# Kernel optimization log

Measured on AMD Instinct MI355X. Metric: run time of the kernel, lower is better.

## Reference

```python
import jax, jax.numpy as jnp
import numpy as np

# Static sizes
B, P, D = 256, 32, 128            # graphs, patches/graph, hidden
N, NS = 200_000, 500_000          # original nodes, combined-subgraph nodes
ES, EO = 1_000_000, 400_000       # combined-subgraph edges, original edges
RW, PRW = 20, 8                   # rw_dim, patch_rw_dim
NL_GNN, NL_MIX = 4, 2
TH, CH = 64, 512                  # mixer token-hidden, channel-hidden
ATOM_V, BOND_V = 128, 8


def seg_sum(x, idx, n):
    return jax.ops.segment_sum(x, idx, num_segments=n)


def seg_mean(x, idx, n):
    s = seg_sum(x, idx, n)
    c = seg_sum(jnp.ones((idx.shape[0], 1), x.dtype), idx, n)
    return s / jnp.maximum(c, 1.0)


def ln(x, g, b):
    m = x.mean(-1, keepdims=True)
    v = x.var(-1, keepdims=True)
    return (x - m) * jax.lax.rsqrt(v + 1e-5) * g + b


def setup_inputs() -> dict:
    key = jax.random.key(0)
    ks = iter(jax.random.split(key, 48))

    def nrm(shape, scale=0.05):
        return jax.random.normal(next(ks), shape, jnp.float32) * scale

    inp = {
        "x_atom": jax.random.randint(next(ks), (N,), 0, ATOM_V),
        "rw_pos_enc": jax.random.normal(next(ks), (N, RW), jnp.float32),
        "edge_attr": jax.random.randint(next(ks), (EO,), 0, BOND_V),
        "nodes_mapper": jax.random.randint(next(ks), (NS,), 0, N),
        "edges_mapper": jax.random.randint(next(ks), (ES,), 0, EO),
        "edge_index": jax.random.randint(next(ks), (2, ES), 0, NS),
        "batch_x": jax.random.randint(next(ks), (NS,), 0, B * P),
        "patch_pe": jax.random.normal(next(ks), (B * P, PRW), jnp.float32),
        "mask": jnp.ones((B, P), dtype=bool),
        # parameters
        "atom_emb": nrm((ATOM_V, D)),
        "bond_emb": nrm((BOND_V, D)),
        "rw_W": nrm((RW, D)), "rw_b": jnp.zeros((D,), jnp.float32),
        "prw_W": nrm((PRW, D)), "prw_b": jnp.zeros((D,), jnp.float32),
        "gnn_W": nrm((NL_GNN, D, D)), "gnn_b": jnp.zeros((NL_GNN, D), jnp.float32),
        "U_W": nrm((NL_GNN - 1, D, D)), "U_b": jnp.zeros((NL_GNN - 1, D), jnp.float32),
        "ln1_g": jnp.ones((NL_MIX, D), jnp.float32), "ln1_b": jnp.zeros((NL_MIX, D), jnp.float32),
        "tW1": nrm((NL_MIX, P, TH)), "tb1": jnp.zeros((NL_MIX, TH), jnp.float32),
        "tW2": nrm((NL_MIX, TH, P)), "tb2": jnp.zeros((NL_MIX, P), jnp.float32),
        "ln2_g": jnp.ones((NL_MIX, D), jnp.float32), "ln2_b": jnp.zeros((NL_MIX, D), jnp.float32),
        "cW1": nrm((NL_MIX, D, CH)), "cb1": jnp.zeros((NL_MIX, CH), jnp.float32),
        "cW2": nrm((NL_MIX, CH, D)), "cb2": jnp.zeros((NL_MIX, D), jnp.float32),
        "oW1": nrm((D, D)), "ob1": jnp.zeros((D,), jnp.float32),
        "oW2": nrm((D, 1)), "ob2": jnp.zeros((1,), jnp.float32),
    }
    return inp


def reference(x_atom, rw_pos_enc, edge_attr, nodes_mapper, edges_mapper, edge_index,
              batch_x, patch_pe, mask, atom_emb, bond_emb, rw_W, rw_b, prw_W, prw_b,
              gnn_W, gnn_b, U_W, U_b, ln1_g, ln1_b, tW1, tb1, tW2, tb2,
              ln2_g, ln2_b, cW1, cb1, cW2, cb2, oW1, ob1, oW2, ob2):
    # node / edge encoders
    x = atom_emb[x_atom] + rw_pos_enc @ rw_W + rw_b          # [N, D]
    e = bond_emb[edge_attr][edges_mapper]                    # [ES, D]
    x = x[nodes_mapper]                                      # [NS, D]
    src, dst = edge_index[0], edge_index[1]

    for i in range(NL_GNN):
        if i > 0:
            # patch-pool -> broadcast back, mix, then sync copies of same node
            sub = seg_mean(x, batch_x, B * P)[batch_x]
            x = x + jax.nn.relu(sub @ U_W[i - 1] + U_b[i - 1])
            x = seg_mean(x, nodes_mapper, N)[nodes_mapper]
        # GINE-style conv: msg = relu(x_src + e), sum-aggregate, MLP, residual
        msg = jax.nn.relu(x[src] + e)                        # [ES, D]
        agg = seg_sum(msg, dst, NS)                          # [NS, D]
        x = x + jax.nn.relu((x + agg) @ gnn_W[i] + gnn_b[i])

    sx = seg_mean(x, batch_x, B * P) + patch_pe @ prw_W + prw_b   # [B*P, D]
    m = sx.reshape(B, P, D)

    for l in range(NL_MIX):
        # token mixing
        y = ln(m, ln1_g[l], ln1_b[l]).transpose(0, 2, 1)     # [B, D, P]
        y = jax.nn.gelu(y @ tW1[l] + tb1[l]) @ tW2[l] + tb2[l]
        m = m + y.transpose(0, 2, 1)
        # channel mixing
        y = ln(m, ln2_g[l], ln2_b[l])
        m = m + (jax.nn.gelu(y @ cW1[l] + cb1[l]) @ cW2[l] + cb2[l])

    mf = mask.astype(jnp.float32)
    pooled = (m * mf[:, :, None]).sum(1) / mf.sum(1, keepdims=True)  # [B, D]
    return jax.nn.relu(pooled @ oW1 + ob1) @ oW2 + ob2              # [B, 1]
```

## Files before the change

kernel.cpp:

```cpp
#include <hip/hip_runtime.h>
#include <hip/hip_bf16.h>
#include <math.h>

#define N_ORIG 200000
#define NS_    500000
#define ES_    1000000
#define B_     256
#define P_     32
#define D_     128
#define BP_    8192
#define RW_    20
#define PRW_   8
#define TH_    64
#define CH_    512

static inline int cdiv_l(long a, long b){ return (int)((a + b - 1) / b); }

typedef unsigned short ushort_t;
typedef __attribute__((ext_vector_type(8))) short gmx_bv8;
typedef __attribute__((ext_vector_type(4))) float gmx_fv4;

__device__ __forceinline__ float b2f(ushort_t u){
    union { unsigned int i; float f; } c; c.i = ((unsigned int)u) << 16; return c.f;
}
__device__ __forceinline__ ushort_t f2b(float f){
    union { float f; unsigned int u; } c; c.f = f;
    unsigned int u = c.u;
    u += 0x7fffu + ((u >> 16) & 1u);
    return (ushort_t)(u >> 16);
}
__device__ __forceinline__ float4 b2f4(ushort4 v){
    return make_float4(b2f(v.x), b2f(v.y), b2f(v.z), b2f(v.w));
}
__device__ __forceinline__ ushort4 f2b4(float4 v){
    ushort4 r; r.x = f2b(v.x); r.y = f2b(v.y); r.z = f2b(v.z); r.w = f2b(v.w); return r;
}

__device__ __forceinline__ float gelu_t(float x){
    float t = tanhf(0.7978845608028654f * (x + 0.044715f * x * x * x));
    return 0.5f * x * (1.0f + t);
}

__global__ void k_breadcrumb(float* __restrict__ out, int n, float v){
    int i = blockIdx.x * 256 + threadIdx.x;
    if (i < n) out[i] = v;
}

__global__ void k_deg_edges(const int* __restrict__ dstv, const int* __restrict__ perm,
                            int* __restrict__ deg){
    int e = blockIdx.x * 256 + threadIdx.x;
    if (e >= ES_) return;
    atomicAdd(&deg[perm[dstv[e]]], 1);
}

__global__ void k_deg_ns(const int* __restrict__ bx, const int* __restrict__ nm,
                         int* __restrict__ pdeg, int* __restrict__ ndeg){
    int i = blockIdx.x * 256 + threadIdx.x;
    if (i >= NS_) return;
    atomicAdd(&pdeg[bx[i]], 1);
    atomicAdd(&ndeg[nm[i]], 1);
}

__global__ __launch_bounds__(256)
void k_scan1(int* __restrict__ a, int* __restrict__ bsum, int n){
    __shared__ int sb[256];
    int tid = threadIdx.x;
    long base = (long)blockIdx.x * 1024 + tid * 4;
    int v0 = 0, v1 = 0, v2 = 0, v3 = 0;
    if (base + 0 < n) v0 = a[base + 0];
    if (base + 1 < n) v1 = a[base + 1];
    if (base + 2 < n) v2 = a[base + 2];
    if (base + 3 < n) v3 = a[base + 3];
    int tsum = v0 + v1 + v2 + v3;
    sb[tid] = tsum;
    __syncthreads();
    for (int o = 1; o < 256; o <<= 1){
        int t = (tid >= o) ? sb[tid - o] : 0;
        __syncthreads();
        sb[tid] += t;
        __syncthreads();
    }
    int excl = sb[tid] - tsum;
    if (tid == 255) bsum[blockIdx.x] = sb[255];
    if (base + 0 < n) a[base + 0] = excl;
    if (base + 1 < n) a[base + 1] = excl + v0;
    if (base + 2 < n) a[base + 2] = excl + v0 + v1;
    if (base + 3 < n) a[base + 3] = excl + v0 + v1 + v2;
}

__global__ __launch_bounds__(512)
void k_scan2(int* __restrict__ bsum, int nb){
    __shared__ int sb[512];
    int tid = threadIdx.x;
    int orig = (tid < nb) ? bsum[tid] : 0;
    sb[tid] = orig;
    __syncthreads();
    for (int o = 1; o < 512; o <<= 1){
        int t = (tid >= o) ? sb[tid - o] : 0;
        __syncthreads();
        sb[tid] += t;
        __syncthreads();
    }
    if (tid < nb) bsum[tid] = sb[tid] - orig;
}

__global__ void k_scan3(int* __restrict__ a, const int* __restrict__ bsum,
                        int* __restrict__ cursor, int n, int total){
    long i = (long)blockIdx.x * 256 + threadIdx.x;
    if (i < n){
        int v = a[i] + bsum[i >> 10];
        a[i] = v;
        cursor[i] = v;
    } else if (i == n){
        a[n] = total;
    }
}

__global__ void k_scatter_ns(const int* __restrict__ bx, const int* __restrict__ nm,
                             int* __restrict__ cur_p, int* __restrict__ cur_n,
                             int* __restrict__ perm, int* __restrict__ bx2,
                             int* __restrict__ nm2, int* __restrict__ plist){
    int i = blockIdx.x * 256 + threadIdx.x;
    if (i >= NS_) return;
    int b = bx[i], n = nm[i];
    int pn = atomicAdd(&cur_n[n], 1);
    perm[i] = pn;
    bx2[pn] = b;
    nm2[pn] = n;
    int pp = atomicAdd(&cur_p[b], 1);
    plist[pp] = pn;
}

__global__ void k_scatter_edges(const int* __restrict__ srcv, const int* __restrict__ dstv,
                                const int* __restrict__ ea, const int* __restrict__ em,
                                const int* __restrict__ nm, const int* __restrict__ perm,
                                int* __restrict__ cursor, int* __restrict__ epack){
    int e = blockIdx.x * 256 + threadIdx.x;
    if (e >= ES_) return;
    int nd = perm[dstv[e]];
    int pos = atomicAdd(&cursor[nd], 1);
    epack[pos] = nm[srcv[e]] | (ea[em[e]] << 18);
}

__global__ void k_encode(const int* __restrict__ xa, const float* __restrict__ rw,
                         const float* __restrict__ aemb, const float* __restrict__ rwW,
                         const float* __restrict__ rwb, ushort_t* __restrict__ xn){
    long i = (long)blockIdx.x * 256 + threadIdx.x;
    if (i >= (long)N_ORIG * 32) return;
    int n = (int)(i >> 5), q = (int)(i & 31);
    const float4* aemb4 = (const float4*)aemb;
    const float4* rwW4  = (const float4*)rwW;
    const float4* rwb4  = (const float4*)rwb;
    float4 v = aemb4[(long)xa[n] * 32 + q];
    float4 bb = rwb4[q];
    v.x += bb.x; v.y += bb.y; v.z += bb.z; v.w += bb.w;
    const float* rr = rw + (long)n * RW_;
    #pragma unroll
    for (int k = 0; k < RW_; k++){
        float rv = rr[k];
        float4 ww = rwW4[k * 32 + q];
        v.x = fmaf(rv, ww.x, v.x); v.y = fmaf(rv, ww.y, v.y);
        v.z = fmaf(rv, ww.z, v.z); v.w = fmaf(rv, ww.w, v.w);
    }
    ((ushort4*)xn)[i] = f2b4(v);
}

__global__ __launch_bounds__(256)
void k_pool_gemm(const ushort_t* __restrict__ xs, const int* __restrict__ prp,
                 const int* __restrict__ plist, const float* __restrict__ W,
                 const float* __restrict__ bvec, ushort_t* __restrict__ out){
    __shared__ char sInB[16 * 256];
    __shared__ int sPrp[17];
    int tid = threadIdx.x;
    int wid = tid >> 6, lane = tid & 63;
    int colA = lane & 15, rgrp = lane >> 4;
    int c0 = 32 * wid + colA, c1 = c0 + 16;
    float bias0 = bvec[c0], bias1 = bvec[c1];
    union { gmx_bv8 v; short s[8]; } bf0[4], bf1[4];
    #pragma unroll
    for (int kb = 0; kb < 4; kb++){
        int kr = kb * 32 + 8 * rgrp;
        #pragma unroll
        for (int j = 0; j < 8; j++){
            bf0[kb].s[j] = (short)f2b(W[(kr + j) * D_ + c0]);
            bf1[kb].s[j] = (short)f2b(W[(kr + j) * D_ + c1]);
        }
    }
    int p0 = blockIdx.x * 16;
    if (tid < 17) sPrp[tid] = prp[p0 + tid];
    __syncthreads();
    const ushort4* xs4 = (const ushort4*)xs;
    #pragma unroll
    for (int it = 0; it < 2; it++){
        int k = tid + it * 256;
        int r = k >> 5, q = k & 31;
        int j0 = sPrp[r], j1 = sPrp[r + 1];
        float4 s0 = make_float4(0.f,0.f,0.f,0.f), s1 = make_float4(0.f,0.f,0.f,0.f);
        int j = j0;
        for (; j + 2 <= j1; j += 2){
            float4 a = b2f4(xs4[(long)plist[j] * 32 + q]);
            float4 b = b2f4(xs4[(long)plist[j + 1] * 32 + q]);
            s0.x += a.x; s0.y += a.y; s0.z += a.z; s0.w += a.w;
            s1.x += b.x; s1.y += b.y; s1.z += b.z; s1.w += b.w;
        }
        if (j < j1){
            float4 a = b2f4(xs4[(long)plist[j] * 32 + q]);
            s0.x += a.x; s0.y += a.y; s0.z += a.z; s0.w += a.w;
        }
        float inv = 1.f / fmaxf((float)(j1 - j0), 1.f);
        float4 v = make_float4((s0.x + s1.x) * inv, (s0.y + s1.y) * inv,
                               (s0.z + s1.z) * inv, (s0.w + s1.w) * inv);
        int off = (r * 256 + q * 8) ^ ((r & 7) << 4);
        *(ushort4*)&sInB[off] = f2b4(v);
    }
    __syncthreads();
    gmx_fv4 acc0 = {0.f,0.f,0.f,0.f}, acc1 = {0.f,0.f,0.f,0.f};
    #pragma unroll
    for (int kb = 0; kb < 4; kb++){
        int kslot = kb * 4 + rgrp;
        gmx_bv8 a = *(const gmx_bv8*)&sInB[(colA * 256 + kslot * 16) ^ ((colA & 7) << 4)];
        acc0 = __builtin_amdgcn_mfma_f32_16x16x32_bf16(a, bf0[kb].v, acc0, 0, 0, 0);
        acc1 = __builtin_amdgcn_mfma_f32_16x16x32_bf16(a, bf1[kb].v, acc1, 0, 0, 0);
    }
    #pragma unroll
    for (int ri = 0; ri < 4; ri++){
        long base = (long)(p0 + rgrp * 4 + ri) * D_;
        out[base + c0] = f2b(fmaxf(acc0[ri] + bias0, 0.f));
        out[base + c1] = f2b(fmaxf(acc1[ri] + bias1, 0.f));
    }
}

__global__ __launch_bounds__(128)
void k_patch_pool_sx(const ushort_t* __restrict__ xs, const int* __restrict__ prp,
                     const int* __restrict__ plist, const float* __restrict__ ppe,
                     const float* __restrict__ pW, const float* __restrict__ pb,
                     float* __restrict__ m){
    int p = blockIdx.x, d = threadIdx.x;
    int j0 = prp[p], j1 = prp[p + 1];
    float s0 = 0.f, s1 = 0.f;
    int j = j0;
    for (; j + 2 <= j1; j += 2){
        s0 += b2f(xs[(long)plist[j] * D_ + d]);
        s1 += b2f(xs[(long)plist[j + 1] * D_ + d]);
    }
    if (j < j1) s0 += b2f(xs[(long)plist[j] * D_ + d]);
    float s = (s0 + s1) / fmaxf((float)(j1 - j0), 1.f) + pb[d];
    #pragma unroll
    for (int k = 0; k < PRW_; k++) s = fmaf(ppe[p * PRW_ + k], pW[k * D_ + d], s);
    m[(long)p * D_ + d] = s;
}

__global__ __launch_bounds__(128)
void k_node_resync(const ushort_t* __restrict__ xs, const ushort_t* __restrict__ subT,
                   const int* __restrict__ bx2, const int* __restrict__ nrp,
                   ushort_t* __restrict__ xn){
    int n = blockIdx.x, d = threadIdx.x;
    int j0 = nrp[n], j1 = nrp[n + 1];
    float s = 0.f;
    int j = j0;
    for (; j + 2 <= j1; j += 2){
        float va = b2f(xs[(long)j * D_ + d]);
        float vb = b2f(xs[(long)(j + 1) * D_ + d]);
        float ua = b2f(subT[(long)bx2[j] * D_ + d]);
        float ub = b2f(subT[(long)bx2[j + 1] * D_ + d]);
        s += va + ua + vb + ub;
    }
    if (j < j1){
        s += b2f(xs[(long)j * D_ + d]) + b2f(subT[(long)bx2[j] * D_ + d]);
    }
    xn[(long)n * D_ + d] = f2b(s / fmaxf((float)(j1 - j0), 1.f));
}

#define CROWS 16

__global__ __launch_bounds__(256)
void k_conv_mfma(const ushort_t* __restrict__ xn, const int* __restrict__ nm2,
                 ushort_t* __restrict__ xout,
                 const int* __restrict__ rp, const int* __restrict__ epack,
                 const float* __restrict__ bond, const float* __restrict__ W,
                 const float* __restrict__ bvec){
    __shared__ char sInB[CROWS * 256];
    __shared__ ushort_t sSelf[CROWS * D_];
    __shared__ int sRp[CROWS + 1];
    __shared__ int sEp[256];
    int tid = threadIdx.x;
    int wid = tid >> 6, lane = tid & 63;
    int colA = lane & 15, rgrp = lane >> 4;
    int c0 = 32 * wid + colA, c1 = c0 + 16;
    float bias0 = bvec[c0], bias1 = bvec[c1];
    union { gmx_bv8 v; short s[8]; } bf0[4], bf1[4];
    #pragma unroll
    for (int kb = 0; kb < 4; kb++){
        int kr = kb * 32 + 8 * rgrp;
        #pragma unroll
        for (int j = 0; j < 8; j++){
            bf0[kb].s[j] = (short)f2b(W[(kr + j) * D_ + c0]);
            bf1[kb].s[j] = (short)f2b(W[(kr + j) * D_ + c1]);
        }
    }
    const ushort4* xn4 = (const ushort4*)xn;
    const float4* bond4 = (const float4*)bond;
    const int ntiles = NS_ / CROWS;
    for (int tile = blockIdx.x; tile < ntiles; tile += gridDim.x){
        int r0 = tile * CROWS;
        if (tid < CROWS + 1) sRp[tid] = rp[r0 + tid];
        __syncthreads();
        int eb0 = sRp[0];
        int ne = sRp[CROWS] - eb0;
        int nc = ne < 256 ? ne : 256;
        for (int k2 = tid; k2 < nc; k2 += 256) sEp[k2] = epack[eb0 + k2];
        __syncthreads();
        #pragma unroll
        for (int it = 0; it < 2; it++){
            int k = tid + it * 256;
            int r = k >> 5, q = k & 31;
            ushort4 selfb = xn4[(long)nm2[r0 + r] * 32 + q];
            *(ushort4*)&sSelf[r * D_ + q * 4] = selfb;
            float4 v = b2f4(selfb);
            int e0 = sRp[r], e1 = sRp[r + 1];
            int e = e0;
            for (; e + 2 <= e1; e += 2){
                int i0 = e - eb0;
                int pk0 = (i0 < 256) ? sEp[i0] : epack[e];
                int pk1 = (i0 + 1 < 256) ? sEp[i0 + 1] : epack[e + 1];
                float4 u0 = b2f4(xn4[(long)(pk0 & 0x3FFFF) * 32 + q]);
                float4 u1 = b2f4(xn4[(long)(pk1 & 0x3FFFF) * 32 + q]);
                float4 b0 = bond4[((pk0 >> 18) & 7) * 32 + q];
                float4 b1 = bond4[((pk1 >> 18) & 7) * 32 + q];
                v.x += fmaxf(u0.x + b0.x, 0.f) + fmaxf(u1.x + b1.x, 0.f);
                v.y += fmaxf(u0.y + b0.y, 0.f) + fmaxf(u1.y + b1.y, 0.f);
                v.z += fmaxf(u0.z + b0.z, 0.f) + fmaxf(u1.z + b1.z, 0.f);
                v.w += fmaxf(u0.w + b0.w, 0.f) + fmaxf(u1.w + b1.w, 0.f);
            }
            if (e < e1){
                int i0 = e - eb0;
                int pk0 = (i0 < 256) ? sEp[i0] : epack[e];
                float4 u0 = b2f4(xn4[(long)(pk0 & 0x3FFFF) * 32 + q]);
                float4 b0 = bond4[((pk0 >> 18) & 7) * 32 + q];
                v.x += fmaxf(u0.x + b0.x, 0.f);
                v.y += fmaxf(u0.y + b0.y, 0.f);
                v.z += fmaxf(u0.z + b0.z, 0.f);
                v.w += fmaxf(u0.w + b0.w, 0.f);
            }
            int off = (r * 256 + q * 8) ^ ((r & 7) << 4);
            *(ushort4*)&sInB[off] = f2b4(v);
        }
        __syncthreads();
        gmx_fv4 acc0 = {0.f,0.f,0.f,0.f}, acc1 = {0.f,0.f,0.f,0.f};
        #pragma unroll
        for (int kb = 0; kb < 4; kb++){
            int kslot = kb * 4 + rgrp;
            gmx_bv8 a = *(const gmx_bv8*)&sInB[(colA * 256 + kslot * 16) ^ ((colA & 7) << 4)];
            acc0 = __builtin_amdgcn_mfma_f32_16x16x32_bf16(a, bf0[kb].v, acc0, 0, 0, 0);
            acc1 = __builtin_amdgcn_mfma_f32_16x16x32_bf16(a, bf1[kb].v, acc1, 0, 0, 0);
        }
        #pragma unroll
        for (int ri = 0; ri < 4; ri++){
            int prow = rgrp * 4 + ri;
            long base = (long)(r0 + prow) * D_;
            float o0 = b2f(sSelf[prow * D_ + c0]) + fmaxf(acc0[ri] + bias0, 0.f);
            float o1 = b2f(sSelf[prow * D_ + c1]) + fmaxf(acc1[ri] + bias1, 0.f);
            xout[base + c0] = f2b(o0);
            xout[base + c1] = f2b(o1);
        }
        __syncthreads();
    }
}

__global__ __launch_bounds__(256)
void k_token_mix(float* __restrict__ m, const float* __restrict__ g, const float* __restrict__ be,
                 const float* __restrict__ tW1, const float* __restrict__ tb1,
                 const float* __restrict__ tW2, const float* __restrict__ tb2){
    __shared__ float sy[P_][D_];
    __shared__ float sh[D_][TH_ + 1];
    int b = blockIdx.x, tid = threadIdx.x;
    float* mb = m + (long)b * P_ * D_;
    int wv = tid >> 6, ln_ = tid & 63;
    for (int r = wv; r < P_; r += 4){
        float v0 = mb[r * D_ + ln_], v1 = mb[r * D_ + 64 + ln_];
        float s = v0 + v1, ss = v0 * v0 + v1 * v1;
        #pragma unroll
        for (int o = 32; o > 0; o >>= 1){ s += __shfl_down(s, o, 64); ss += __shfl_down(ss, o, 64); }
        s = __shfl(s, 0, 64); ss = __shfl(ss, 0, 64);
        float mu = s * (1.f / 128.f);
        float var = ss * (1.f / 128.f) - mu * mu;
        float rs = rsqrtf(var + 1e-5f);
        sy[r][ln_]      = (v0 - mu) * rs * g[ln_]      + be[ln_];
        sy[r][64 + ln_] = (v1 - mu) * rs * g[64 + ln_] + be[64 + ln_];
    }
    __syncthreads();
    for (int o = tid; o < D_ * TH_; o += 256){
        int t = o & 63, d = o >> 6;
        float a = tb1[t];
        #pragma unroll
        for (int p = 0; p < P_; p++) a = fmaf(sy[p][d], tW1[p * TH_ + t], a);
        sh[d][t] = gelu_t(a);
    }
    __syncthreads();
    for (int o = tid; o < P_ * D_; o += 256){
        int d = o & 127, p = o >> 7;
        float a = tb2[p];
        #pragma unroll
        for (int t = 0; t < TH_; t++) a = fmaf(sh[d][t], tW2[t * P_ + p], a);
        mb[p * D_ + d] += a;
    }
}

__global__ __launch_bounds__(256)
void k_channel_mix(float* __restrict__ m, const float* __restrict__ g, const float* __restrict__ be,
                   const float* __restrict__ cW1, const float* __restrict__ cb1,
                   const float* __restrict__ cW2, const float* __restrict__ cb2){
    __shared__ float sy[16][D_];
    __shared__ float sh[16][CH_ + 1];
    int r0 = blockIdx.x * 16, tid = threadIdx.x;
    int wv = tid >> 6, ln_ = tid & 63;
    for (int r = wv; r < 16; r += 4){
        float v0 = m[(long)(r0 + r) * D_ + ln_], v1 = m[(long)(r0 + r) * D_ + 64 + ln_];
        float s = v0 + v1, ss = v0 * v0 + v1 * v1;
        #pragma unroll
        for (int o = 32; o > 0; o >>= 1){ s += __shfl_down(s, o, 64); ss += __shfl_down(ss, o, 64); }
        s = __shfl(s, 0, 64); ss = __shfl(ss, 0, 64);
        float mu = s * (1.f / 128.f);
        float var = ss * (1.f / 128.f) - mu * mu;
        float rs = rsqrtf(var + 1e-5f);
        sy[r][ln_]      = (v0 - mu) * rs * g[ln_]      + be[ln_];
        sy[r][64 + ln_] = (v1 - mu) * rs * g[64 + ln_] + be[64 + ln_];
    }
    __syncthreads();
    #pragma unroll
    for (int th = 0; th < 2; th++){
        int t = tid + th * 256;
        float acc[16];
        #pragma unroll
        for (int r = 0; r < 16; r++) acc[r] = cb1[t];
        for (int k = 0; k < D_; k++){
            float w = cW1[k * CH_ + t];
            #pragma unroll
            for (int r = 0; r < 16; r++) acc[r] = fmaf(sy[r][k], w, acc[r]);
        }
        #pragma unroll
        for (int r = 0; r < 16; r++) sh[r][t] = gelu_t(acc[r]);
    }
    __syncthreads();
    {
        int d = tid & 127, rbase = tid >> 7;
        float acc[8];
        #pragma unroll
        for (int q = 0; q < 8; q++) acc[q] = 0.f;
        for (int t = 0; t < CH_; t++){
            float w = cW2[t * D_ + d];
            #pragma unroll
            for (int q = 0; q < 8; q++) acc[q] = fmaf(sh[rbase + 2 * q][t], w, acc[q]);
        }
        float cb = cb2[d];
        #pragma unroll
        for (int q = 0; q < 8; q++){
            int row = r0 + rbase + 2 * q;
            m[(long)row * D_ + d] += acc[q] + cb;
        }
    }
}

__global__ __launch_bounds__(128)
void k_final(const float* __restrict__ m, const float* __restrict__ oW1, const float* __restrict__ ob1,
             const float* __restrict__ oW2, const float* __restrict__ ob2, float* __restrict__ out){
    __shared__ float sp[D_];
    __shared__ float red[128];
    int b = blockIdx.x, tid = threadIdx.x;
    float a = 0.f;
    for (int p = 0; p < P_; p++) a += m[(long)b * P_ * D_ + p * D_ + tid];
    sp[tid] = a * (1.0f / P_);
    __syncthreads();
    float h = ob1[tid];
    for (int d = 0; d < D_; d++) h = fmaf(sp[d], oW1[d * D_ + tid], h);
    h = fmaxf(h, 0.f) * oW2[tid];
    red[tid] = h;
    __syncthreads();
    for (int s = 64; s > 0; s >>= 1){
        if (tid < s) red[tid] += red[tid + s];
        __syncthreads();
    }
    if (tid == 0) out[b] = red[0] + ob2[0];
}

extern "C" void kernel_launch(void* const* d_in, const int* in_sizes, int n_in,
                              void* d_out, int out_size, void* d_ws, size_t ws_size,
                              hipStream_t stream){
    const int*   x_atom       = (const int*)  d_in[0];
    const float* rw_pe        = (const float*)d_in[1];
    const int*   edge_attr    = (const int*)  d_in[2];
    const int*   nodes_mapper = (const int*)  d_in[3];
    const int*   edges_mapper = (const int*)  d_in[4];
    const int*   edge_index   = (const int*)  d_in[5];
    const int*   batch_x      = (const int*)  d_in[6];
    const float* patch_pe     = (const float*)d_in[7];
    const float* atom_emb = (const float*)d_in[9];
    const float* bond_emb = (const float*)d_in[10];
    const float* rw_W  = (const float*)d_in[11];
    const float* rw_b  = (const float*)d_in[12];
    const float* prw_W = (const float*)d_in[13];
    const float* prw_b = (const float*)d_in[14];
    const float* gnn_W = (const float*)d_in[15];
    const float* gnn_b = (const float*)d_in[16];
    const float* U_W   = (const float*)d_in[17];
    const float* U_b   = (const float*)d_in[18];
    const float* ln1_g = (const float*)d_in[19];
    const float* ln1_b = (const float*)d_in[20];
    const float* tW1   = (const float*)d_in[21];
    const float* tb1   = (const float*)d_in[22];
    const float* tW2   = (const float*)d_in[23];
    const float* tb2   = (const float*)d_in[24];
    const float* ln2_g = (const float*)d_in[25];
    const float* ln2_b = (const float*)d_in[26];
    const float* cW1   = (const float*)d_in[27];
    const float* cb1   = (const float*)d_in[28];
    const float* cW2   = (const float*)d_in[29];
    const float* cb2   = (const float*)d_in[30];
    const float* oW1   = (const float*)d_in[31];
    const float* ob1   = (const float*)d_in[32];
    const float* oW2   = (const float*)d_in[33];
    const float* ob2   = (const float*)d_in[34];

    const int* srcv = edge_index;
    const int* dstv = edge_index + ES_;

    char* w = (char*)d_ws;
    size_t offXS  = 0;
    size_t offXN  = offXS  + (size_t)NS_ * D_ * 2;
    size_t offRP  = offXN  + (size_t)N_ORIG * D_ * 2;
    size_t offEP  = offRP  + 2000064;
    size_t offPRP = offEP  + (size_t)ES_ * 4;
    size_t offNRP = offPRP + 32832;
    size_t offPL  = offNRP + 800064;
    size_t offPERM= offPL  + (size_t)NS_ * 4;
    size_t offBX2 = offPERM+ (size_t)NS_ * 4;
    size_t offNM2 = offBX2 + (size_t)NS_ * 4;
    size_t offBS  = offNM2 + (size_t)NS_ * 4;
    size_t offST  = offBS  + 2048;
    size_t offM   = offST  + (size_t)BP_ * D_ * 2;
    size_t needed = offM   + (size_t)BP_ * D_ * 4;

    if (ws_size < needed){
        k_breadcrumb<<<cdiv_l(out_size, 256), 256, 0, stream>>>((float*)d_out, out_size,
                                                                (float)(ws_size >> 20));
        return;
    }

    k_breadcrumb<<<cdiv_l(out_size, 256), 256, 0, stream>>>((float*)d_out, out_size, 7.0f);

    ushort_t* xs = (ushort_t*)(w + offXS);
    ushort_t* xn = (ushort_t*)(w + offXN);
    int* rp    = (int*)(w + offRP);
    int* ep    = (int*)(w + offEP);
    int* prp   = (int*)(w + offPRP);
    int* nrp   = (int*)(w + offNRP);
    int* plist = (int*)(w + offPL);
    int* perm  = (int*)(w + offPERM);
    int* bx2   = (int*)(w + offBX2);
    int* nm2   = (int*)(w + offNM2);
    int* bsum  = (int*)(w + offBS);
    ushort_t* subT = (ushort_t*)(w + offST);
    float*    mbuf = (float*)(w + offM);
    int* cur_e = (int*)(w + offXS);
    int* cur_p = (int*)(w + offXS + 4194304);
    int* cur_n = (int*)(w + offXS + 8388608);

    const int TPB = 256;

    hipMemsetAsync(prp, 0, 32832, stream);
    hipMemsetAsync(nrp, 0, 800064, stream);
    k_deg_ns<<<cdiv_l(NS_, TPB), TPB, 0, stream>>>(batch_x, nodes_mapper, prp, nrp);
    k_scan1<<<cdiv_l(BP_, 1024), TPB, 0, stream>>>(prp, bsum, BP_);
    k_scan2<<<1, 512, 0, stream>>>(bsum, cdiv_l(BP_, 1024));
    k_scan3<<<cdiv_l(BP_ + 1, TPB), TPB, 0, stream>>>(prp, bsum, cur_p, BP_, NS_);
    k_scan1<<<cdiv_l(N_ORIG, 1024), TPB, 0, stream>>>(nrp, bsum, N_ORIG);
    k_scan2<<<1, 512, 0, stream>>>(bsum, cdiv_l(N_ORIG, 1024));
    k_scan3<<<cdiv_l(N_ORIG + 1, TPB), TPB, 0, stream>>>(nrp, bsum, cur_n, N_ORIG, NS_);
    k_scatter_ns<<<cdiv_l(NS_, TPB), TPB, 0, stream>>>(batch_x, nodes_mapper, cur_p, cur_n,
                                                       perm, bx2, nm2, plist);
    hipMemsetAsync(rp, 0, 2000064, stream);
    k_deg_edges<<<cdiv_l(ES_, TPB), TPB, 0, stream>>>(dstv, perm, rp);
    k_scan1<<<cdiv_l(NS_, 1024), TPB, 0, stream>>>(rp, bsum, NS_);
    k_scan2<<<1, 512, 0, stream>>>(bsum, cdiv_l(NS_, 1024));
    k_scan3<<<cdiv_l(NS_ + 1, TPB), TPB, 0, stream>>>(rp, bsum, cur_e, NS_, ES_);
    k_scatter_edges<<<cdiv_l(ES_, TPB), TPB, 0, stream>>>(srcv, dstv, edge_attr, edges_mapper,
                                                          nodes_mapper, perm, cur_e, ep);

    k_encode<<<cdiv_l((long)N_ORIG * 32, TPB), TPB, 0, stream>>>(x_atom, rw_pe, atom_emb,
                                                                 rw_W, rw_b, xn);

    for (int i = 0; i < 4; i++){
        if (i > 0){
            k_pool_gemm<<<BP_ / 16, TPB, 0, stream>>>(xs, prp, plist,
                                                      U_W + (i - 1) * D_ * D_,
                                                      U_b + (i - 1) * D_, subT);
            k_node_resync<<<N_ORIG, 128, 0, stream>>>(xs, subT, bx2, nrp, xn);
        }
        k_conv_mfma<<<2048, TPB, 0, stream>>>(xn, nm2, xs, rp, ep, bond_emb,
                                              gnn_W + i * D_ * D_, gnn_b + i * D_);
    }

    k_patch_pool_sx<<<BP_, 128, 0, stream>>>(xs, prp, plist, patch_pe, prw_W, prw_b, mbuf);

    for (int l = 0; l < 2; l++){
        k_token_mix<<<B_, TPB, 0, stream>>>(mbuf, ln1_g + l * D_, ln1_b + l * D_,
                                            tW1 + l * P_ * TH_, tb1 + l * TH_,
                                            tW2 + l * TH_ * P_, tb2 + l * P_);
        k_channel_mix<<<BP_ / 16, TPB, 0, stream>>>(mbuf, ln2_g + l * D_, ln2_b + l * D_,
                                                    cW1 + l * D_ * CH_, cb1 + l * CH_,
                                                    cW2 + l * CH_ * D_, cb2 + l * D_);
    }
    k_final<<<B_, 128, 0, stream>>>(mbuf, oW1, ob1, oW2, ob2, (float*)d_out);
}
```

Measured before the change: 1.625 ms.

## Widen conv blocks to 512 threads, cache permuted edge dst, unroll pooling loops

The GINE conv kernel now runs 512-thread blocks, with each wave owning 16 output columns and each thread gathering one row-quad per tile. The grid grows to 4096 blocks. This is meant to raise parallelism in the gather stage and cut per-thread register pressure, at the cost of each wave holding a duplicate load of the A operand. Separately, the permuted destination index is saved once during degree counting so the edge scatter no longer reads perm[dstv[e]] a second time, which costs an extra 4 MB buffer. The patch pooling loops are unrolled by four to keep more independent gathers in flight.

```diff
diff --git a/kernel.cpp b/kernel.cpp
--- a/kernel.cpp
+++ b/kernel.cpp
@@ -47,10 +47,12 @@
 }
 
 __global__ void k_deg_edges(const int* __restrict__ dstv, const int* __restrict__ perm,
-                            int* __restrict__ deg){
+                            int* __restrict__ deg, int* __restrict__ dst2){
     int e = blockIdx.x * 256 + threadIdx.x;
     if (e >= ES_) return;
-    atomicAdd(&deg[perm[dstv[e]]], 1);
+    int nd = perm[dstv[e]];
+    dst2[e] = nd;
+    atomicAdd(&deg[nd], 1);
 }
 
 __global__ void k_deg_ns(const int* __restrict__ bx, const int* __restrict__ nm,
@@ -131,14 +133,13 @@
     plist[pp] = pn;
 }
 
-__global__ void k_scatter_edges(const int* __restrict__ srcv, const int* __restrict__ dstv,
+__global__ void k_scatter_edges(const int* __restrict__ srcv, const int* __restrict__ dst2,
                                 const int* __restrict__ ea, const int* __restrict__ em,
-                                const int* __restrict__ nm, const int* __restrict__ perm,
+                                const int* __restrict__ nm,
                                 int* __restrict__ cursor, int* __restrict__ epack){
     int e = blockIdx.x * 256 + threadIdx.x;
     if (e >= ES_) return;
-    int nd = perm[dstv[e]];
-    int pos = atomicAdd(&cursor[nd], 1);
+    int pos = atomicAdd(&cursor[dst2[e]], 1);
     epack[pos] = nm[srcv[e]] | (ea[em[e]] << 18);
 }
 
@@ -196,20 +197,27 @@
         int r = k >> 5, q = k & 31;
         int j0 = sPrp[r], j1 = sPrp[r + 1];
         float4 s0 = make_float4(0.f,0.f,0.f,0.f), s1 = make_float4(0.f,0.f,0.f,0.f);
+        float4 s2 = make_float4(0.f,0.f,0.f,0.f), s3 = make_float4(0.f,0.f,0.f,0.f);
         int j = j0;
-        for (; j + 2 <= j1; j += 2){
+        for (; j + 4 <= j1; j += 4){
             float4 a = b2f4(xs4[(long)plist[j] * 32 + q]);
             float4 b = b2f4(xs4[(long)plist[j + 1] * 32 + q]);
+            float4 c = b2f4(xs4[(long)plist[j + 2] * 32 + q]);
+            float4 d = b2f4(xs4[(long)plist[j + 3] * 32 + q]);
             s0.x += a.x; s0.y += a.y; s0.z += a.z; s0.w += a.w;
             s1.x += b.x; s1.y += b.y; s1.z += b.z; s1.w += b.w;
-        }
-        if (j < j1){
+            s2.x += c.x; s2.y += c.y; s2.z += c.z; s2.w += c.w;
+            s3.x += d.x; s3.y += d.y; s3.z += d.z; s3.w += d.w;
+        }
+        for (; j < j1; j++){
             float4 a = b2f4(xs4[(long)plist[j] * 32 + q]);
             s0.x += a.x; s0.y += a.y; s0.z += a.z; s0.w += a.w;
         }
         float inv = 1.f / fmaxf((float)(j1 - j0), 1.f);
-        float4 v = make_float4((s0.x + s1.x) * inv, (s0.y + s1.y) * inv,
-                               (s0.z + s1.z) * inv, (s0.w + s1.w) * inv);
+        float4 v = make_float4((s0.x + s1.x + s2.x + s3.x) * inv,
+                               (s0.y + s1.y + s2.y + s3.y) * inv,
+                               (s0.z + s1.z + s2.z + s3.z) * inv,
+                               (s0.w + s1.w + s2.w + s3.w) * inv);
         int off = (r * 256 + q * 8) ^ ((r & 7) << 4);
         *(ushort4*)&sInB[off] = f2b4(v);
     }
@@ -237,14 +245,16 @@
                      float* __restrict__ m){
     int p = blockIdx.x, d = threadIdx.x;
     int j0 = prp[p], j1 = prp[p + 1];
-    float s0 = 0.f, s1 = 0.f;
+    float s0 = 0.f, s1 = 0.f, s2 = 0.f, s3 = 0.f;
     int j = j0;
-    for (; j + 2 <= j1; j += 2){
+    for (; j + 4 <= j1; j += 4){
         s0 += b2f(xs[(long)plist[j] * D_ + d]);
         s1 += b2f(xs[(long)plist[j + 1] * D_ + d]);
-    }
-    if (j < j1) s0 += b2f(xs[(long)plist[j] * D_ + d]);
-    float s = (s0 + s1) / fmaxf((float)(j1 - j0), 1.f) + pb[d];
+        s2 += b2f(xs[(long)plist[j + 2] * D_ + d]);
+        s3 += b2f(xs[(long)plist[j + 3] * D_ + d]);
+    }
+    for (; j < j1; j++) s0 += b2f(xs[(long)plist[j] * D_ + d]);
+    float s = (s0 + s1 + s2 + s3) / fmaxf((float)(j1 - j0), 1.f) + pb[d];
     #pragma unroll
     for (int k = 0; k < PRW_; k++) s = fmaf(ppe[p * PRW_ + k], pW[k * D_ + d], s);
     m[(long)p * D_ + d] = s;
@@ -273,7 +283,7 @@
 
 #define CROWS 16
 
-__global__ __launch_bounds__(256)
+__global__ __launch_bounds__(512)
 void k_conv_mfma(const ushort_t* __restrict__ xn, const int* __restrict__ nm2,
                  ushort_t* __restrict__ xout,
                  const int* __restrict__ rp, const int* __restrict__ epack,
@@ -286,21 +296,21 @@
     int tid = threadIdx.x;
     int wid = tid >> 6, lane = tid & 63;
     int colA = lane & 15, rgrp = lane >> 4;
-    int c0 = 32 * wid + colA, c1 = c0 + 16;
-    float bias0 = bvec[c0], bias1 = bvec[c1];
-    union { gmx_bv8 v; short s[8]; } bf0[4], bf1[4];
+    int c0 = 16 * wid + colA;
+    float bias0 = bvec[c0];
+    union { gmx_bv8 v; short s[8]; } bf0[4];
     #pragma unroll
     for (int kb = 0; kb < 4; kb++){
         int kr = kb * 32 + 8 * rgrp;
         #pragma unroll
         for (int j = 0; j < 8; j++){
             bf0[kb].s[j] = (short)f2b(W[(kr + j) * D_ + c0]);
-            bf1[kb].s[j] = (short)f2b(W[(kr + j) * D_ + c1]);
         }
     }
     const ushort4* xn4 = (const ushort4*)xn;
     const float4* bond4 = (const float4*)bond;
     const int ntiles = NS_ / CROWS;
+    int r = tid >> 5, q = tid & 31;
     for (int tile = blockIdx.x; tile < ntiles; tile += gridDim.x){
         int r0 = tile * CROWS;
         if (tid < CROWS + 1) sRp[tid] = rp[r0 + tid];
@@ -308,12 +318,9 @@
         int eb0 = sRp[0];
         int ne = sRp[CROWS] - eb0;
         int nc = ne < 256 ? ne : 256;
-        for (int k2 = tid; k2 < nc; k2 += 256) sEp[k2] = epack[eb0 + k2];
-        __syncthreads();
-        #pragma unroll
-        for (int it = 0; it < 2; it++){
-            int k = tid + it * 256;
-            int r = k >> 5, q = k & 31;
+        for (int k2 = tid; k2 < nc; k2 += 512) sEp[k2] = epack[eb0 + k2];
+        __syncthreads();
+        {
             ushort4 selfb = xn4[(long)nm2[r0 + r] * 32 + q];
             *(ushort4*)&sSelf[r * D_ + q * 4] = selfb;
             float4 v = b2f4(selfb);
@@ -346,22 +353,19 @@
             *(ushort4*)&sInB[off] = f2b4(v);
         }
         __syncthreads();
-        gmx_fv4 acc0 = {0.f,0.f,0.f,0.f}, acc1 = {0.f,0.f,0.f,0.f};
+        gmx_fv4 acc = {0.f,0.f,0.f,0.f};
         #pragma unroll
         for (int kb = 0; kb < 4; kb++){
             int kslot = kb * 4 + rgrp;
             gmx_bv8 a = *(const gmx_bv8*)&sInB[(colA * 256 + kslot * 16) ^ ((colA & 7) << 4)];
-            acc0 = __builtin_amdgcn_mfma_f32_16x16x32_bf16(a, bf0[kb].v, acc0, 0, 0, 0);
-            acc1 = __builtin_amdgcn_mfma_f32_16x16x32_bf16(a, bf1[kb].v, acc1, 0, 0, 0);
+            acc = __builtin_amdgcn_mfma_f32_16x16x32_bf16(a, bf0[kb].v, acc, 0, 0, 0);
         }
         #pragma unroll
         for (int ri = 0; ri < 4; ri++){
             int prow = rgrp * 4 + ri;
             long base = (long)(r0 + prow) * D_;
-            float o0 = b2f(sSelf[prow * D_ + c0]) + fmaxf(acc0[ri] + bias0, 0.f);
-            float o1 = b2f(sSelf[prow * D_ + c1]) + fmaxf(acc1[ri] + bias1, 0.f);
+            float o0 = b2f(sSelf[prow * D_ + c0]) + fmaxf(acc[ri] + bias0, 0.f);
             xout[base + c0] = f2b(o0);
-            xout[base + c1] = f2b(o1);
         }
         __syncthreads();
     }
@@ -529,7 +533,8 @@
     size_t offXN  = offXS  + (size_t)NS_ * D_ * 2;
     size_t offRP  = offXN  + (size_t)N_ORIG * D_ * 2;
     size_t offEP  = offRP  + 2000064;
-    size_t offPRP = offEP  + (size_t)ES_ * 4;
+    size_t offDST2= offEP  + (size_t)ES_ * 4;
+    size_t offPRP = offDST2+ (size_t)ES_ * 4;
     size_t offNRP = offPRP + 32832;
     size_t offPL  = offNRP + 800064;
     size_t offPERM= offPL  + (size_t)NS_ * 4;
@@ -552,6 +557,7 @@
     ushort_t* xn = (ushort_t*)(w + offXN);
     int* rp    = (int*)(w + offRP);
     int* ep    = (int*)(w + offEP);
+    int* dst2  = (int*)(w + offDST2);
     int* prp   = (int*)(w + offPRP);
     int* nrp   = (int*)(w + offNRP);
     int* plist = (int*)(w + offPL);
@@ -579,12 +585,12 @@
     k_scatter_ns<<<cdiv_l(NS_, TPB), TPB, 0, stream>>>(batch_x, nodes_mapper, cur_p, cur_n,
                                                        perm, bx2, nm2, plist);
     hipMemsetAsync(rp, 0, 2000064, stream);
-    k_deg_edges<<<cdiv_l(ES_, TPB), TPB, 0, stream>>>(dstv, perm, rp);
+    k_deg_edges<<<cdiv_l(ES_, TPB), TPB, 0, stream>>>(dstv, perm, rp, dst2);
     k_scan1<<<cdiv_l(NS_, 1024), TPB, 0, stream>>>(rp, bsum, NS_);
     k_scan2<<<1, 512, 0, stream>>>(bsum, cdiv_l(NS_, 1024));
     k_scan3<<<cdiv_l(NS_ + 1, TPB), TPB, 0, stream>>>(rp, bsum, cur_e, NS_, ES_);
-    k_scatter_edges<<<cdiv_l(ES_, TPB), TPB, 0, stream>>>(srcv, dstv, edge_attr, edges_mapper,
-                                                          nodes_mapper, perm, cur_e, ep);
+    k_scatter_edges<<<cdiv_l(ES_, TPB), TPB, 0, stream>>>(srcv, dst2, edge_attr, edges_mapper,
+                                                          nodes_mapper, cur_e, ep);
 
     k_encode<<<cdiv_l((long)N_ORIG * 32, TPB), TPB, 0, stream>>>(x_atom, rw_pe, atom_emb,
                                                                  rw_W, rw_b, xn);
@@ -596,7 +602,7 @@
                                                       U_b + (i - 1) * D_, subT);
             k_node_resync<<<N_ORIG, 128, 0, stream>>>(xs, subT, bx2, nrp, xn);
         }
-        k_conv_mfma<<<2048, TPB, 0, stream>>>(xn, nm2, xs, rp, ep, bond_emb,
+        k_conv_mfma<<<4096, 512, 0, stream>>>(xn, nm2, xs, rp, ep, bond_emb,
                                               gnn_W + i * D_ * D_, gnn_b + i * D_);
     }
 
```

Measured after the change: 1.558 ms. 1.04x faster.
